# Optimization experiments

Measured on AMD Instinct MI355X. Metric: run time of the kernel, lower is better.

The kernel has to match this reference:

```python
import jax, jax.numpy as jnp
import numpy as np

S2_CH, DEM_CH, OUT_CH = 256, 64, 256
B, H, W = 4, 64, 64


def setup_inputs() -> dict:
    key = jax.random.key(0)
    ks = jax.random.split(key, 8)
    x_s2 = jax.random.normal(ks[0], (B, S2_CH, H, W), dtype=jnp.float32)
    x_dem = jax.random.normal(ks[1], (B, DEM_CH, H, W), dtype=jnp.float32)
    # 1x1 conv weights collapse to [out_ch, in_ch] matrices + bias
    Wq = jax.random.normal(ks[2], (OUT_CH, S2_CH), dtype=jnp.float32) * (S2_CH ** -0.5)
    bq = jnp.zeros((OUT_CH,), dtype=jnp.float32)
    Wk = jax.random.normal(ks[3], (OUT_CH, DEM_CH), dtype=jnp.float32) * (DEM_CH ** -0.5)
    bk = jnp.zeros((OUT_CH,), dtype=jnp.float32)
    Wv = jax.random.normal(ks[4], (OUT_CH, DEM_CH), dtype=jnp.float32) * (DEM_CH ** -0.5)
    bv = jnp.zeros((OUT_CH,), dtype=jnp.float32)
    return {"x_s2": x_s2, "x_dem": x_dem, "Wq": Wq, "bq": bq,
            "Wk": Wk, "bk": bk, "Wv": Wv, "bv": bv}


def reference(x_s2, x_dem, Wq, bq, Wk, bk, Wv, bv):
    b, c, h, w = x_s2.shape
    n = h * w
    xs = x_s2.reshape(b, c, n)                      # [b, s2_ch, n]
    xd = x_dem.reshape(b, x_dem.shape[1], n)        # [b, dem_ch, n]
    # 1x1 convs == per-pixel GEMMs
    q = jnp.einsum('oc,bcn->bon', Wq, xs) + bq[:, None]   # [b, out_ch, n]
    k = jnp.einsum('oc,bcn->bon', Wk, xd) + bk[:, None]   # [b, out_ch, n]
    v = jnp.einsum('oc,bcn->bon', Wv, xd) + bv[:, None]   # [b, out_ch, n]
    scale = q.shape[1] ** -0.5
    # attn[b,i,j] = softmax_j( k[b,:,i] . q[b,:,j] * scale )
    attn = jax.nn.softmax(jnp.einsum('bci,bcj->bij', k, q) * scale, axis=-1)
    out = jnp.einsum('bci,bij->bcj', v, attn).reshape(b, -1, h, w)
    return out + x_s2
```

## Files before the change

### kernel.cpp

```cpp
#include <hip/hip_runtime.h>
#include <hip/hip_bf16.h>
#include <cstdint>

#define B_  4
#define N_  4096
#define C_  256
#define CD_ 64

typedef unsigned short ushort_t;
typedef unsigned char uchar_t;
typedef __bf16 bf16x8 __attribute__((ext_vector_type(8)));
typedef float f32x4 __attribute__((ext_vector_type(4)));
typedef unsigned int u32x4 __attribute__((ext_vector_type(4)));

typedef const __attribute__((address_space(1))) void* gas_t;
typedef __attribute__((address_space(3))) void* las_t;

static constexpr float SCALE_LOG2E = 0.09016844005556021f;
static constexpr float SCALE_K8 = 0.3606737602222408f;
static constexpr float SCALE_Q8 = 0.25f;
static constexpr float VSCALE = 8192.0f;
static constexpr float VSCALE_INV = 1.0f / 8192.0f;

__device__ __forceinline__ ushort_t f2bf(float x) {
    union { float f; unsigned u; } v; v.f = x;
    unsigned u = v.u;
    unsigned r = (u + 0x7fffu + ((u >> 16) & 1u)) >> 16;
    return (ushort_t)r;
}

__device__ __forceinline__ uchar_t f2fp8(float x) {
    return (uchar_t)(__builtin_amdgcn_cvt_pk_fp8_f32(x, x, 0, false) & 0xff);
}

__device__ __forceinline__ bf16x8 ld_bf8(const ushort_t* p) {
    return *reinterpret_cast<const bf16x8*>(p);
}

__global__ __launch_bounds__(256, 4)
void proj_q_mfma(const float* __restrict__ X, const float* __restrict__ W,
                 const float* __restrict__ bias, ushort_t* __restrict__ dst,
                 uchar_t* __restrict__ dst8, int Cin) {
    __shared__ ushort_t sX[128][72];
    __shared__ ushort_t sW[64][72];
    const int tid = threadIdx.x;
    const int lane = tid & 63, g = lane >> 4, c16 = lane & 15;
    const int w = tid >> 6, wi = w >> 1, wj = w & 1;
    const int b = blockIdx.z, nb = blockIdx.x * 128, ob = blockIdx.y * 64;
    f32x4 acc[4][2];
#pragma unroll
    for (int nt = 0; nt < 4; ++nt)
#pragma unroll
        for (int ot = 0; ot < 2; ++ot) acc[nt][ot] = (f32x4){0.f, 0.f, 0.f, 0.f};

    const int cr = tid >> 5;
    const int n0 = (tid & 31) * 4;

    for (int k0 = 0; k0 < Cin; k0 += 64) {
#pragma unroll
        for (int p = 0; p < 8; ++p) {
            const int c = p * 8 + cr;
            float4 xv = *(const float4*)(X + ((size_t)b * Cin + k0 + c) * N_ + nb + n0);
            sX[n0 + 0][c] = f2bf(xv.x);
            sX[n0 + 1][c] = f2bf(xv.y);
            sX[n0 + 2][c] = f2bf(xv.z);
            sX[n0 + 3][c] = f2bf(xv.w);
        }
        {
            const int o = tid >> 2, cq = (tid & 3) * 16;
            const float* wsrc = W + (size_t)(ob + o) * Cin + k0 + cq;
            alignas(16) ushort_t tmp[16];
#pragma unroll
            for (int q = 0; q < 16; ++q) tmp[q] = f2bf(wsrc[q]);
            *(uint4*)&sW[o][cq]     = *(uint4*)&tmp[0];
            *(uint4*)&sW[o][cq + 8] = *(uint4*)&tmp[8];
        }
        __syncthreads();
#pragma unroll
        for (int ks = 0; ks < 2; ++ks) {
            bf16x8 af[4], bfr[2];
#pragma unroll
            for (int nt = 0; nt < 4; ++nt)
                af[nt] = *(const bf16x8*)&sX[wi * 64 + nt * 16 + c16][ks * 32 + g * 8];
#pragma unroll
            for (int ot = 0; ot < 2; ++ot)
                bfr[ot] = *(const bf16x8*)&sW[wj * 32 + ot * 16 + c16][ks * 32 + g * 8];
#pragma unroll
            for (int nt = 0; nt < 4; ++nt)
#pragma unroll
                for (int ot = 0; ot < 2; ++ot)
                    acc[nt][ot] = __builtin_amdgcn_mfma_f32_16x16x32_bf16(af[nt], bfr[ot], acc[nt][ot], 0, 0, 0);
        }
        __syncthreads();
    }
#pragma unroll
    for (int ot = 0; ot < 2; ++ot) {
        const int o = ob + wj * 32 + ot * 16 + c16;
        const float bia = bias[o];
#pragma unroll
        for (int nt = 0; nt < 4; ++nt) {
#pragma unroll
            for (int r = 0; r < 4; ++r) {
                const int n = nb + wi * 64 + nt * 16 + g * 4 + r;
                const float v = acc[nt][ot][r] + bia;
                if (dst8 != nullptr)
                    dst8[((size_t)b * N_ + n) * C_ + o] = f2fp8(v * SCALE_Q8);
                else
                    dst[((size_t)b * N_ + n) * C_ + o] = f2bf(v);
            }
        }
    }
}

__global__ __launch_bounds__(256, 4)
void proj_kv_mfma(const float* __restrict__ X, const float* __restrict__ Wk,
                  const float* __restrict__ bk, const float* __restrict__ Wv,
                  const float* __restrict__ bv, ushort_t* __restrict__ Kt,
                  uchar_t* __restrict__ Kt8, ushort_t* __restrict__ Vm) {
    __shared__ ushort_t sX[128][72];
    __shared__ ushort_t sWk[64][72];
    __shared__ ushort_t sWv[64][72];
    const int tid = threadIdx.x;
    const int lane = tid & 63, g = lane >> 4, c16 = lane & 15;
    const int w = tid >> 6;
    const int b = blockIdx.z, nb = blockIdx.x * 128, ob = blockIdx.y * 64;

    {
        const int cr = tid >> 5, n0 = (tid & 31) * 4;
#pragma unroll
        for (int p = 0; p < 8; ++p) {
            const int c = p * 8 + cr;
            float4 xv = *(const float4*)(X + ((size_t)b * CD_ + c) * N_ + nb + n0);
            sX[n0 + 0][c] = f2bf(xv.x);
            sX[n0 + 1][c] = f2bf(xv.y);
            sX[n0 + 2][c] = f2bf(xv.z);
            sX[n0 + 3][c] = f2bf(xv.w);
        }
        const int o = tid >> 2, cq = (tid & 3) * 16;
        alignas(16) ushort_t tk[16], tv[16];
        const float* ksrc = Wk + (size_t)(ob + o) * CD_ + cq;
        const float* vsrc = Wv + (size_t)(ob + o) * CD_ + cq;
#pragma unroll
        for (int q = 0; q < 16; ++q) { tk[q] = f2bf(ksrc[q]); tv[q] = f2bf(vsrc[q]); }
        *(uint4*)&sWk[o][cq]     = *(uint4*)&tk[0];
        *(uint4*)&sWk[o][cq + 8] = *(uint4*)&tk[8];
        *(uint4*)&sWv[o][cq]     = *(uint4*)&tv[0];
        *(uint4*)&sWv[o][cq + 8] = *(uint4*)&tv[8];
    }
    __syncthreads();
    {
        const int wi = w >> 1, wj = w & 1;
        f32x4 acc[4][2];
#pragma unroll
        for (int nt = 0; nt < 4; ++nt)
#pragma unroll
            for (int ot = 0; ot < 2; ++ot) acc[nt][ot] = (f32x4){0.f, 0.f, 0.f, 0.f};
#pragma unroll
        for (int ks = 0; ks < 2; ++ks) {
            bf16x8 af[4], bfr[2];
#pragma unroll
            for (int nt = 0; nt < 4; ++nt)
                af[nt] = *(const bf16x8*)&sX[wi * 64 + nt * 16 + c16][ks * 32 + g * 8];
#pragma unroll
            for (int ot = 0; ot < 2; ++ot)
                bfr[ot] = *(const bf16x8*)&sWk[wj * 32 + ot * 16 + c16][ks * 32 + g * 8];
#pragma unroll
            for (int nt = 0; nt < 4; ++nt)
#pragma unroll
                for (int ot = 0; ot < 2; ++ot)
                    acc[nt][ot] = __builtin_amdgcn_mfma_f32_16x16x32_bf16(af[nt], bfr[ot], acc[nt][ot], 0, 0, 0);
        }
#pragma unroll
        for (int ot = 0; ot < 2; ++ot) {
            const int o = ob + wj * 32 + ot * 16 + c16;
            const float bia = bk[o];
#pragma unroll
            for (int nt = 0; nt < 4; ++nt)
#pragma unroll
                for (int r = 0; r < 4; ++r) {
                    const int n = nb + wi * 64 + nt * 16 + g * 4 + r;
                    const float v = acc[nt][ot][r] + bia;
                    if (Kt8 != nullptr)
                        Kt8[((size_t)b * N_ + n) * C_ + o] = f2fp8(v * SCALE_K8);
                    else
                        Kt[((size_t)b * N_ + n) * C_ + o] = f2bf(v * SCALE_LOG2E);
                }
        }
    }
    {
        const int ow = w & 1, nw = w >> 1;
        f32x4 acc[2][4];
#pragma unroll
        for (int mt = 0; mt < 2; ++mt)
#pragma unroll
            for (int nt = 0; nt < 4; ++nt) acc[mt][nt] = (f32x4){0.f, 0.f, 0.f, 0.f};
#pragma unroll
        for (int ks = 0; ks < 2; ++ks) {
            bf16x8 af[2], bfr[4];
#pragma unroll
            for (int mt = 0; mt < 2; ++mt)
                af[mt] = *(const bf16x8*)&sWv[ow * 32 + mt * 16 + c16][ks * 32 + g * 8];
#pragma unroll
            for (int nt = 0; nt < 4; ++nt)
                bfr[nt] = *(const bf16x8*)&sX[nw * 64 + nt * 16 + c16][ks * 32 + g * 8];
#pragma unroll
            for (int mt = 0; mt < 2; ++mt)
#pragma unroll
                for (int nt = 0; nt < 4; ++nt)
                    acc[mt][nt] = __builtin_amdgcn_mfma_f32_16x16x32_bf16(af[mt], bfr[nt], acc[mt][nt], 0, 0, 0);
        }
#pragma unroll
        for (int mt = 0; mt < 2; ++mt) {
            const float4 bi4 = *(const float4*)(bv + ob + ow * 32 + mt * 16 + g * 4);
            const float bia[4] = {bi4.x, bi4.y, bi4.z, bi4.w};
#pragma unroll
            for (int nt = 0; nt < 4; ++nt) {
                const int n = nb + nw * 64 + nt * 16 + c16;
#pragma unroll
                for (int r = 0; r < 4; ++r) {
                    const int o = ob + ow * 32 + mt * 16 + g * 4 + r;
                    Vm[((size_t)b * C_ + o) * N_ + n] = f2bf(acc[mt][nt][r] + bia[r]);
                }
            }
        }
    }
}

__global__ __launch_bounds__(256, 4)
void stats_fp8_kernel(const uchar_t* __restrict__ Kt8, const uchar_t* __restrict__ Qt8,
                      uchar_t* __restrict__ PT8, float* __restrict__ lpart) {
    __shared__ uchar_t smem8[32768];
    uchar_t* sp8 = smem8;
    float* lsum = (float*)(smem8 + 18432);
    const int tid = threadIdx.x;
    const int lane = tid & 63, g = lane >> 4, c16 = lane & 15;
    const int w = tid >> 6, wi = w >> 1, wj = w & 1;
    const int b = blockIdx.z;
    const int ib = blockIdx.y * 128, jb = blockIdx.x * 128;
    f32x4 acc[4][4];
#pragma unroll
    for (int mt = 0; mt < 4; ++mt)
#pragma unroll
        for (int nt = 0; nt < 4; ++nt) acc[mt][nt] = (f32x4){0.f, 0.f, 0.f, 0.f};

    const int srow = tid >> 2;
    const int sc = tid & 3;

    auto stage = [&](int kc, int dbase) {
#pragma unroll
        for (int q = 0; q < 2; ++q) {
            const int row = q * 64 + srow;
            const int gc = sc ^ ((row >> 1) & 3);
            const uchar_t* srcA = Kt8 + ((size_t)(b * N_ + ib + row)) * C_ + kc * 64 + gc * 16;
            const uchar_t* srcB = Qt8 + ((size_t)(b * N_ + jb + row)) * C_ + kc * 64 + gc * 16;
            __builtin_amdgcn_global_load_lds((gas_t)srcA, (las_t)&smem8[dbase + (q * 256 + tid) * 16], 16, 0, 0);
            __builtin_amdgcn_global_load_lds((gas_t)srcB, (las_t)&smem8[dbase + 8192 + (q * 256 + tid) * 16], 16, 0, 0);
        }
    };

    stage(0, 0);
    __syncthreads();
    for (int t = 0; t < 4; ++t) {
        const int dbase = (t & 1) * 16384;
        if (t < 3) stage(t + 1, 16384 - dbase);
#pragma unroll
        for (int ks = 0; ks < 2; ++ks) {
            const int sp = ks * 2 + (g >> 1);
            const int bo = (g & 1) * 8;
            long af[4], bf[4];
#pragma unroll
            for (int mt = 0; mt < 4; ++mt) {
                const int row = wi * 64 + mt * 16 + c16;
                af[mt] = *(const long*)&smem8[dbase + row * 64 + ((sp ^ ((row >> 1) & 3)) * 16) + bo];
            }
#pragma unroll
            for (int nt = 0; nt < 4; ++nt) {
                const int row = wj * 64 + nt * 16 + c16;
                bf[nt] = *(const long*)&smem8[dbase + 8192 + row * 64 + ((sp ^ ((row >> 1) & 3)) * 16) + bo];
            }
#pragma unroll
            for (int mt = 0; mt < 4; ++mt)
#pragma unroll
                for (int nt = 0; nt < 4; ++nt)
                    acc[mt][nt] = __builtin_amdgcn_mfma_f32_16x16x32_fp8_fp8(af[mt], bf[nt], acc[mt][nt], 0, 0, 0);
        }
        __syncthreads();
    }
    const float sh = 3.0f;
#pragma unroll
    for (int mt = 0; mt < 4; ++mt) {
        float rs[4] = {0.f, 0.f, 0.f, 0.f};
#pragma unroll
        for (int nt = 0; nt < 4; ++nt) {
            float e0 = __builtin_amdgcn_exp2f(acc[mt][nt][0] - sh);
            float e1 = __builtin_amdgcn_exp2f(acc[mt][nt][1] - sh);
            float e2 = __builtin_amdgcn_exp2f(acc[mt][nt][2] - sh);
            float e3 = __builtin_amdgcn_exp2f(acc[mt][nt][3] - sh);
            rs[0] += e0; rs[1] += e1; rs[2] += e2; rs[3] += e3;
            int pk = __builtin_amdgcn_cvt_pk_fp8_f32(e0, e1, 0, false);
            pk = __builtin_amdgcn_cvt_pk_fp8_f32(e2, e3, pk, true);
            const int jl = wj * 64 + nt * 16 + c16;
            const int il = wi * 64 + mt * 16 + g * 4;
            *(int*)&sp8[jl * 144 + il] = pk;
        }
#pragma unroll
        for (int r = 0; r < 4; ++r) {
            float s = rs[r];
            s += __shfl_xor(s, 1, 64);
            s += __shfl_xor(s, 2, 64);
            s += __shfl_xor(s, 4, 64);
            s += __shfl_xor(s, 8, 64);
            if (c16 == 0)
                lsum[wj * 128 + wi * 64 + mt * 16 + g * 4 + r] = s;
        }
    }
    __syncthreads();
    {
        const int chb = tid & 7;
        const int rb = tid >> 3;
#pragma unroll
        for (int r = 0; r < 4; ++r) {
            const int jl = r * 32 + rb;
            u32x4 v = *(const u32x4*)&sp8[jl * 144 + chb * 16];
            __builtin_nontemporal_store(v,
                (u32x4*)(PT8 + ((size_t)(b * N_ + jb + jl)) * N_ + ib + chb * 16));
        }
        if (tid < 128) {
            float tot = lsum[tid] + lsum[128 + tid];
            lpart[((size_t)(b * 32 + (jb >> 7))) * N_ + ib + tid] = tot;
        }
    }
}

__global__ __launch_bounds__(256, 4)
void stats_kernel(const ushort_t* __restrict__ Kt, const ushort_t* __restrict__ Qt,
                  float* __restrict__ l) {
    __shared__ ushort_t smem[16384];
    uchar_t* smem8 = (uchar_t*)smem;
    const int tid = threadIdx.x;
    const int lane = tid & 63, g = lane >> 4, c16 = lane & 15;
    const int w = tid >> 6, wi = w >> 1, wj = w & 1;
    const int b = blockIdx.z;
    const int ib = blockIdx.y * 128, jb = blockIdx.x * 128;
    f32x4 acc[4][4];
#pragma unroll
    for (int mt = 0; mt < 4; ++mt)
#pragma unroll
        for (int nt = 0; nt < 4; ++nt) acc[mt][nt] = (f32x4){0.f, 0.f, 0.f, 0.f};

    const int srow = tid >> 2;
    const int sc = tid & 3;

    auto stage = [&](int kc, int dbase) {
#pragma unroll
        for (int q = 0; q < 2; ++q) {
            const int row = q * 64 + srow;
            const int gc = sc ^ ((row >> 1) & 3);
            const ushort_t* srcA = Kt + ((size_t)(b * N_ + ib + row)) * C_ + kc * 32 + gc * 8;
            const ushort_t* srcB = Qt + ((size_t)(b * N_ + jb + row)) * C_ + kc * 32 + gc * 8;
            __builtin_amdgcn_global_load_lds((gas_t)srcA, (las_t)&smem8[dbase + (q * 256 + tid) * 16], 16, 0, 0);
            __builtin_amdgcn_global_load_lds((gas_t)srcB, (las_t)&smem8[dbase + 8192 + (q * 256 + tid) * 16], 16, 0, 0);
        }
    };

    stage(0, 0);
    __syncthreads();
    for (int t = 0; t < 8; ++t) {
        const int dbase = (t & 1) * 16384;
        if (t < 7) stage(t + 1, 16384 - dbase);
        bf16x8 af[4], bf[4];
#pragma unroll
        for (int mt = 0; mt < 4; ++mt) {
            const int row = wi * 64 + mt * 16 + c16;
            af[mt] = *(const bf16x8*)&smem8[dbase + row * 64 + ((g ^ ((row >> 1) & 3)) * 16)];
        }
#pragma unroll
        for (int nt = 0; nt < 4; ++nt) {
            const int row = wj * 64 + nt * 16 + c16;
            bf[nt] = *(const bf16x8*)&smem8[dbase + 8192 + row * 64 + ((g ^ ((row >> 1) & 3)) * 16)];
        }
#pragma unroll
        for (int mt = 0; mt < 4; ++mt)
#pragma unroll
            for (int nt = 0; nt < 4; ++nt)
                acc[mt][nt] = __builtin_amdgcn_mfma_f32_16x16x32_bf16(af[mt], bf[nt], acc[mt][nt], 0, 0, 0);
        __syncthreads();
    }
#pragma unroll
    for (int mt = 0; mt < 4; ++mt) {
        float rs[4] = {0.f, 0.f, 0.f, 0.f};
#pragma unroll
        for (int nt = 0; nt < 4; ++nt) {
            rs[0] += __builtin_amdgcn_exp2f(acc[mt][nt][0]);
            rs[1] += __builtin_amdgcn_exp2f(acc[mt][nt][1]);
            rs[2] += __builtin_amdgcn_exp2f(acc[mt][nt][2]);
            rs[3] += __builtin_amdgcn_exp2f(acc[mt][nt][3]);
        }
#pragma unroll
        for (int r = 0; r < 4; ++r) {
            float s = rs[r];
            s += __shfl_xor(s, 1, 64);
            s += __shfl_xor(s, 2, 64);
            s += __shfl_xor(s, 4, 64);
            s += __shfl_xor(s, 8, 64);
            if (c16 == 0)
                atomicAdd(l + (size_t)b * N_ + ib + wi * 64 + mt * 16 + g * 4 + r, s);
        }
    }
}

__global__ void reduce_l_kernel(const float* __restrict__ lpart, float* __restrict__ l) {
    const int b = blockIdx.y;
    const int i = (blockIdx.x * 256 + threadIdx.x) * 4;
    float4 s = {0.f, 0.f, 0.f, 0.f};
#pragma unroll
    for (int jt = 0; jt < 32; ++jt) {
        float4 p = *(const float4*)(lpart + ((size_t)(b * 32 + jt)) * N_ + i);
        s.x += p.x; s.y += p.y; s.z += p.z; s.w += p.w;
    }
    *(float4*)(l + (size_t)b * N_ + i) = s;
}

__global__ void scale_v_kernel(const ushort_t* __restrict__ Vm, const float* __restrict__ l,
                               uchar_t* __restrict__ Vs) {
    const int i = (blockIdx.x * 256 + threadIdx.x) * 8;
    const int c = blockIdx.y, b = blockIdx.z;
    float4 l0 = *(const float4*)(l + (size_t)b * N_ + i);
    float4 l1 = *(const float4*)(l + (size_t)b * N_ + i + 4);
    float r[8] = {__builtin_amdgcn_rcpf(l0.x), __builtin_amdgcn_rcpf(l0.y),
                  __builtin_amdgcn_rcpf(l0.z), __builtin_amdgcn_rcpf(l0.w),
                  __builtin_amdgcn_rcpf(l1.x), __builtin_amdgcn_rcpf(l1.y),
                  __builtin_amdgcn_rcpf(l1.z), __builtin_amdgcn_rcpf(l1.w)};
    const size_t off = ((size_t)(b * C_ + c)) * N_ + i;
    uint4 v = *(const uint4*)(Vm + off);
    unsigned vw[4] = {v.x, v.y, v.z, v.w};
    float f[8];
#pragma unroll
    for (int q = 0; q < 4; ++q) {
        union { unsigned u; float fl; } lo, hi;
        lo.u = (vw[q] & 0xffffu) << 16;
        hi.u = vw[q] & 0xffff0000u;
        f[q * 2 + 0] = lo.fl * r[q * 2 + 0] * VSCALE;
        f[q * 2 + 1] = hi.fl * r[q * 2 + 1] * VSCALE;
    }
    int d0 = __builtin_amdgcn_cvt_pk_fp8_f32(f[0], f[1], 0, false);
    d0 = __builtin_amdgcn_cvt_pk_fp8_f32(f[2], f[3], d0, true);
    int d1 = __builtin_amdgcn_cvt_pk_fp8_f32(f[4], f[5], 0, false);
    d1 = __builtin_amdgcn_cvt_pk_fp8_f32(f[6], f[7], d1, true);
    uint2 o; o.x = (unsigned)d0; o.y = (unsigned)d1;
    *(uint2*)(Vs + off) = o;
}

__global__ __launch_bounds__(512, 4)
void gemm_out2_kernel(const uchar_t* __restrict__ A ,
                      const uchar_t* __restrict__ Bm ,
                      const float* __restrict__ R ,
                      float* __restrict__ out) {
    __shared__ uchar_t smem[73728];
    const int tid = threadIdx.x;
    const int lane = tid & 63, g = lane >> 4, c16 = lane & 15;
    const int w = tid >> 6;
    const int cw = w * 32;
    const int b = blockIdx.y;
    const int jb = blockIdx.x * 32;

    f32x4 acc[2][2];
#pragma unroll
    for (int mt = 0; mt < 2; ++mt)
#pragma unroll
        for (int nt = 0; nt < 2; ++nt) acc[mt][nt] = (f32x4){0.f, 0.f, 0.f, 0.f};

    const int sch = tid & 7;

    auto stage = [&](int k0, int dbase) {
#pragma unroll
        for (int q = 0; q < 4; ++q) {
            const int slot = q * 512 + tid;
            const int row = slot >> 3;
            const int gc = sch ^ (row & 7);
            const uchar_t* src = A + ((size_t)(b * C_ + row)) * N_ + k0 + gc * 16;
            __builtin_amdgcn_global_load_lds((gas_t)src, (las_t)&smem[dbase + slot * 16], 16, 0, 0);
        }
        if (tid < 256) {
            const int row = tid >> 3;
            const int gc = sch ^ (row & 7);
            const uchar_t* src = Bm + ((size_t)(b * N_ + jb + row)) * N_ + k0 + gc * 16;
            __builtin_amdgcn_global_load_lds((gas_t)src, (las_t)&smem[dbase + 32768 + tid * 16], 16, 0, 2);
        }
    };

    stage(0, 0);
    __syncthreads();
    for (int t = 0; t < 32; ++t) {
        const int dbase = (t & 1) * 36864;
        if (t < 31) stage((t + 1) * 128, 36864 - dbase);
        const uchar_t* sA = &smem[dbase];
        const uchar_t* sB = &smem[dbase + 32768];
#pragma unroll
        for (int ks = 0; ks < 4; ++ks) {
            const int lc = ks * 2 + (g >> 1);
            const int bo = (g & 1) * 8;
            long af[2], bfg[2];
#pragma unroll
            for (int mt = 0; mt < 2; ++mt) {
                const int row = cw + mt * 16 + c16;
                af[mt] = *(const long*)&sA[row * 128 + ((lc ^ (row & 7)) * 16) + bo];
            }
#pragma unroll
            for (int nt = 0; nt < 2; ++nt) {
                const int row = nt * 16 + c16;
                bfg[nt] = *(const long*)&sB[row * 128 + ((lc ^ (row & 7)) * 16) + bo];
            }
#pragma unroll
            for (int mt = 0; mt < 2; ++mt)
#pragma unroll
                for (int nt = 0; nt < 2; ++nt)
                    acc[mt][nt] = __builtin_amdgcn_mfma_f32_16x16x32_fp8_fp8(af[mt], bfg[nt], acc[mt][nt], 0, 0, 0);
        }
        __syncthreads();
    }
#pragma unroll
    for (int mt = 0; mt < 2; ++mt)
#pragma unroll
        for (int r = 0; r < 4; ++r) {
            const int c = cw + mt * 16 + g * 4 + r;
            const size_t rowoff = ((size_t)(b * C_ + c)) * N_ + jb;
#pragma unroll
            for (int nt = 0; nt < 2; ++nt) {
                const int j = nt * 16 + c16;
                float rv = __builtin_nontemporal_load(&R[rowoff + j]);
                __builtin_nontemporal_store(rv + acc[mt][nt][r] * VSCALE_INV,
                                            &out[rowoff + j]);
            }
        }
}

__global__ __launch_bounds__(512, 4)
void out_kernel(const ushort_t* __restrict__ Kt, const ushort_t* __restrict__ Qt,
                const ushort_t* __restrict__ V, const float* __restrict__ l,
                float* __restrict__ dout) {
    __shared__ ushort_t sQ[64][264];
    __shared__ ushort_t sP[64][264];
    const int tid = threadIdx.x;
    const int w = tid >> 6, lane = tid & 63, g = lane >> 4, c16 = lane & 15;
    const int b = blockIdx.z;
    const int jb = blockIdx.x * 64;
    const int ibase = blockIdx.y * 2048;
    {
        const int jl = tid >> 3, cp = (tid & 7) * 32;
        const ushort_t* src = Qt + ((size_t)(b * N_ + jb + jl)) * C_ + cp;
        uint4 a0 = *(const uint4*)(src);
        uint4 a1 = *(const uint4*)(src + 8);
        uint4 a2 = *(const uint4*)(src + 16);
        uint4 a3 = *(const uint4*)(src + 24);
        *(uint4*)&sQ[jl][cp + 0]  = a0;
        *(uint4*)&sQ[jl][cp + 8]  = a1;
        *(uint4*)&sQ[jl][cp + 16] = a2;
        *(uint4*)&sQ[jl][cp + 24] = a3;
    }
    f32x4 acc[2][4];
#pragma unroll
    for (int mt = 0; mt < 2; ++mt)
#pragma unroll
        for (int nt = 0; nt < 4; ++nt) acc[mt][nt] = (f32x4){0.f, 0.f, 0.f, 0.f};

    const int bw = w * 32;

    for (int ic = 0; ic < 8; ++ic) {
        const int i0 = ibase + ic * 256;
        float rv[2][4];
#pragma unroll
        for (int mt = 0; mt < 2; ++mt) {
            float4 lr = *(const float4*)(l + (size_t)b * N_ + i0 + bw + mt * 16 + g * 4);
            rv[mt][0] = __builtin_amdgcn_logf(lr.x);
            rv[mt][1] = __builtin_amdgcn_logf(lr.y);
            rv[mt][2] = __builtin_amdgcn_logf(lr.z);
            rv[mt][3] = __builtin_amdgcn_logf(lr.w);
        }
        __syncthreads();
        f32x4 sa[2][4];
#pragma unroll
        for (int mt = 0; mt < 2; ++mt)
#pragma unroll
            for (int nt = 0; nt < 4; ++nt) sa[mt][nt] = (f32x4){0.f, 0.f, 0.f, 0.f};
#pragma unroll
        for (int k = 0; k < 8; ++k) {
            bf16x8 av[2];
#pragma unroll
            for (int mt = 0; mt < 2; ++mt)
                av[mt] = ld_bf8(Kt + ((size_t)(b * N_ + i0 + bw + mt * 16 + c16)) * C_ + k * 32 + g * 8);
#pragma unroll
            for (int nt = 0; nt < 4; ++nt) {
                bf16x8 bv = *(const bf16x8*)&sQ[nt * 16 + c16][k * 32 + g * 8];
#pragma unroll
                for (int mt = 0; mt < 2; ++mt)
                    sa[mt][nt] = __builtin_amdgcn_mfma_f32_16x16x32_bf16(av[mt], bv, sa[mt][nt], 0, 0, 0);
            }
        }
#pragma unroll
        for (int mt = 0; mt < 2; ++mt)
#pragma unroll
            for (int nt = 0; nt < 4; ++nt) {
                const int j = nt * 16 + c16;
                unsigned p0 = f2bf(__builtin_amdgcn_exp2f(sa[mt][nt][0] - rv[mt][0]));
                unsigned p1 = f2bf(__builtin_amdgcn_exp2f(sa[mt][nt][1] - rv[mt][1]));
                unsigned p2 = f2bf(__builtin_amdgcn_exp2f(sa[mt][nt][2] - rv[mt][2]));
                unsigned p3 = f2bf(__builtin_amdgcn_exp2f(sa[mt][nt][3] - rv[mt][3]));
                uint2 pk; pk.x = p0 | (p1 << 16); pk.y = p2 | (p3 << 16);
                *(uint2*)&sP[j][bw + mt * 16 + g * 4] = pk;
            }
        __syncthreads();
#pragma unroll
        for (int ks = 0; ks < 8; ++ks) {
            bf16x8 va[2];
#pragma unroll
            for (int mt = 0; mt < 2; ++mt)
                va[mt] = ld_bf8(V + ((size_t)(b * C_ + bw + mt * 16 + c16)) * N_ + i0 + ks * 32 + g * 8);
#pragma unroll
            for (int nt = 0; nt < 4; ++nt) {
                bf16x8 pb = *(const bf16x8*)&sP[nt * 16 + c16][ks * 32 + g * 8];
#pragma unroll
                for (int mt = 0; mt < 2; ++mt)
                    acc[mt][nt] = __builtin_amdgcn_mfma_f32_16x16x32_bf16(va[mt], pb, acc[mt][nt], 0, 0, 0);
            }
        }
    }
#pragma unroll
    for (int mt = 0; mt < 2; ++mt)
#pragma unroll
        for (int nt = 0; nt < 4; ++nt)
#pragma unroll
            for (int r = 0; r < 4; ++r) {
                const int c = bw + mt * 16 + g * 4 + r;
                const int j = jb + nt * 16 + c16;
                atomicAdd(dout + ((size_t)b * C_ + c) * N_ + j, acc[mt][nt][r]);
            }
}

extern "C" void kernel_launch(void* const* d_in, const int* in_sizes, int n_in,
                              void* d_out, int out_size, void* d_ws, size_t ws_size,
                              hipStream_t stream) {
    const float* x_s2  = (const float*)d_in[0];
    const float* x_dem = (const float*)d_in[1];
    const float* Wq = (const float*)d_in[2];
    const float* bq = (const float*)d_in[3];
    const float* Wk = (const float*)d_in[4];
    const float* bk = (const float*)d_in[5];
    const float* Wv = (const float*)d_in[6];
    const float* bv = (const float*)d_in[7];
    float* out = (float*)d_out;

    const size_t MiB = 1024 * 1024;
    char* ws = (char*)d_ws;
    ushort_t* Qt = (ushort_t*)(ws);
    uchar_t*  Qt8 = (uchar_t*)(ws);
    ushort_t* Kt = (ushort_t*)(ws + 8  * MiB);
    uchar_t*  Kt8 = (uchar_t*)(ws + 8 * MiB);
    ushort_t* Vm = (ushort_t*)(ws + 16 * MiB);
    uchar_t*  Vs = (uchar_t*) (ws + 24 * MiB);
    float*    lp = (float*)   (ws + 24 * MiB);
    float*    lv = (float*)   (ws + 28 * MiB);
    uchar_t*  PT = (uchar_t*) (ws + 29 * MiB);
    const bool bigws = ws_size >= 93 * MiB;

    if (!bigws) {
        hipMemsetAsync(lv, 0, (size_t)B_ * N_ * sizeof(float), stream);
        hipMemcpyAsync(out, x_s2, (size_t)B_ * C_ * N_ * sizeof(float),
                       hipMemcpyDeviceToDevice, stream);
    }

    proj_q_mfma<<<dim3(N_ / 128, C_ / 64, B_), 256, 0, stream>>>(
        x_s2, Wq, bq, Qt, bigws ? Qt8 : (uchar_t*)nullptr, C_);
    proj_kv_mfma<<<dim3(N_ / 128, C_ / 64, B_), 256, 0, stream>>>(
        x_dem, Wk, bk, Wv, bv, Kt, bigws ? Kt8 : (uchar_t*)nullptr, Vm);
    if (bigws) {
        stats_fp8_kernel<<<dim3(N_ / 128, N_ / 128, B_), 256, 0, stream>>>(Kt8, Qt8, PT, lp);
        reduce_l_kernel<<<dim3(N_ / 1024, B_), 256, 0, stream>>>(lp, lv);
        scale_v_kernel<<<dim3(N_ / 2048, C_, B_), 256, 0, stream>>>(Vm, lv, Vs);
        gemm_out2_kernel<<<dim3(N_ / 32, B_), 512, 0, stream>>>(Vs, PT, x_s2, out);
    } else {
        stats_kernel<<<dim3(N_ / 128, N_ / 128, B_), 256, 0, stream>>>(Kt, Qt, lv);
        out_kernel<<<dim3(N_ / 64, 2, B_), 512, 0, stream>>>(Kt, Qt, Vm, lv, out);
    }
}
```

Baseline: 198.7 us.

## Permute K-dimension byte order in fp8 operands to enable 16-byte LDS fragment reads

The fp8 Q, K, P and V tensors are now written with their reduction-dimension bytes permuted so that each lane's two consecutive MFMA k-steps sit in one contiguous 16-byte chunk. The score and output GEMMs then issue one 128-bit LDS read per fragment pair instead of two 64-bit reads, halving the LDS read instruction count. The producers (projection epilogues, softmax P store, V scaling) must apply matching permutations, and any mismatch would silently corrupt the result.

```diff
diff --git a/kernel.cpp b/kernel.cpp
--- a/kernel.cpp
+++ b/kernel.cpp
@@ -12,6 +12,7 @@
 typedef __bf16 bf16x8 __attribute__((ext_vector_type(8)));
 typedef float f32x4 __attribute__((ext_vector_type(4)));
 typedef unsigned int u32x4 __attribute__((ext_vector_type(4)));
+typedef long longx2 __attribute__((ext_vector_type(2)));
 
 typedef const __attribute__((address_space(1))) void* gas_t;
 typedef __attribute__((address_space(3))) void* las_t;
@@ -35,6 +36,13 @@
 
 __device__ __forceinline__ bf16x8 ld_bf8(const ushort_t* p) {
     return *reinterpret_cast<const bf16x8*>(p);
+}
+
+__device__ __forceinline__ int perm16(int s) {
+    return (((s & 3) | ((s >> 1) & 4)) << 4) | ((s & 4) << 1);
+}
+__device__ __forceinline__ int perm8(int s) {
+    return ((s & 3) << 4) | ((s & 4) << 1);
 }
 
 __global__ __launch_bounds__(256, 4)
@@ -97,6 +105,7 @@
     for (int ot = 0; ot < 2; ++ot) {
         const int o = ob + wj * 32 + ot * 16 + c16;
         const float bia = bias[o];
+        const int o_p = (o & ~63) | perm8((o >> 3) & 7) | (o & 7);
 #pragma unroll
         for (int nt = 0; nt < 4; ++nt) {
 #pragma unroll
@@ -104,7 +113,7 @@
                 const int n = nb + wi * 64 + nt * 16 + g * 4 + r;
                 const float v = acc[nt][ot][r] + bia;
                 if (dst8 != nullptr)
-                    dst8[((size_t)b * N_ + n) * C_ + o] = f2fp8(v * SCALE_Q8);
+                    dst8[((size_t)b * N_ + n) * C_ + o_p] = f2fp8(v * SCALE_Q8);
                 else
                     dst[((size_t)b * N_ + n) * C_ + o] = f2bf(v);
             }
@@ -174,6 +183,7 @@
         for (int ot = 0; ot < 2; ++ot) {
             const int o = ob + wj * 32 + ot * 16 + c16;
             const float bia = bk[o];
+            const int o_p = (o & ~63) | perm8((o >> 3) & 7) | (o & 7);
 #pragma unroll
             for (int nt = 0; nt < 4; ++nt)
 #pragma unroll
@@ -181,7 +191,7 @@
                     const int n = nb + wi * 64 + nt * 16 + g * 4 + r;
                     const float v = acc[nt][ot][r] + bia;
                     if (Kt8 != nullptr)
-                        Kt8[((size_t)b * N_ + n) * C_ + o] = f2fp8(v * SCALE_K8);
+                        Kt8[((size_t)b * N_ + n) * C_ + o_p] = f2fp8(v * SCALE_K8);
                     else
                         Kt[((size_t)b * N_ + n) * C_ + o] = f2bf(v * SCALE_LOG2E);
                 }
@@ -263,27 +273,24 @@
     for (int t = 0; t < 4; ++t) {
         const int dbase = (t & 1) * 16384;
         if (t < 3) stage(t + 1, 16384 - dbase);
-#pragma unroll
-        for (int ks = 0; ks < 2; ++ks) {
-            const int sp = ks * 2 + (g >> 1);
-            const int bo = (g & 1) * 8;
-            long af[4], bf[4];
-#pragma unroll
-            for (int mt = 0; mt < 4; ++mt) {
-                const int row = wi * 64 + mt * 16 + c16;
-                af[mt] = *(const long*)&smem8[dbase + row * 64 + ((sp ^ ((row >> 1) & 3)) * 16) + bo];
-            }
-#pragma unroll
-            for (int nt = 0; nt < 4; ++nt) {
-                const int row = wj * 64 + nt * 16 + c16;
-                bf[nt] = *(const long*)&smem8[dbase + 8192 + row * 64 + ((sp ^ ((row >> 1) & 3)) * 16) + bo];
-            }
+        longx2 a2[4], b2[4];
+#pragma unroll
+        for (int mt = 0; mt < 4; ++mt) {
+            const int row = wi * 64 + mt * 16 + c16;
+            a2[mt] = *(const longx2*)&smem8[dbase + row * 64 + ((g ^ ((row >> 1) & 3)) * 16)];
+        }
+#pragma unroll
+        for (int nt = 0; nt < 4; ++nt) {
+            const int row = wj * 64 + nt * 16 + c16;
+            b2[nt] = *(const longx2*)&smem8[dbase + 8192 + row * 64 + ((g ^ ((row >> 1) & 3)) * 16)];
+        }
+#pragma unroll
+        for (int ks = 0; ks < 2; ++ks)
 #pragma unroll
             for (int mt = 0; mt < 4; ++mt)
 #pragma unroll
                 for (int nt = 0; nt < 4; ++nt)
-                    acc[mt][nt] = __builtin_amdgcn_mfma_f32_16x16x32_fp8_fp8(af[mt], bf[nt], acc[mt][nt], 0, 0, 0);
-        }
+                    acc[mt][nt] = __builtin_amdgcn_mfma_f32_16x16x32_fp8_fp8(a2[mt][ks], b2[nt][ks], acc[mt][nt], 0, 0, 0);
         __syncthreads();
     }
     const float sh = 3.0f;
@@ -301,7 +308,8 @@
             pk = __builtin_amdgcn_cvt_pk_fp8_f32(e2, e3, pk, true);
             const int jl = wj * 64 + nt * 16 + c16;
             const int il = wi * 64 + mt * 16 + g * 4;
-            *(int*)&sp8[jl * 144 + il] = pk;
+            const int il_p = perm16(il >> 3) | (il & 7);
+            *(int*)&sp8[jl * 144 + il_p] = pk;
         }
 #pragma unroll
         for (int r = 0; r < 4; ++r) {
@@ -448,7 +456,8 @@
     int d1 = __builtin_amdgcn_cvt_pk_fp8_f32(f[4], f[5], 0, false);
     d1 = __builtin_amdgcn_cvt_pk_fp8_f32(f[6], f[7], d1, true);
     uint2 o; o.x = (unsigned)d0; o.y = (unsigned)d1;
-    *(uint2*)(Vs + off) = o;
+    const int i_p = (i & ~127) | perm16((i >> 3) & 15);
+    *(uint2*)(Vs + ((size_t)(b * C_ + c)) * N_ + i_p) = o;
 }
 
 __global__ __launch_bounds__(512, 4)
@@ -496,27 +505,28 @@
         if (t < 31) stage((t + 1) * 128, 36864 - dbase);
         const uchar_t* sA = &smem[dbase];
         const uchar_t* sB = &smem[dbase + 32768];
-#pragma unroll
-        for (int ks = 0; ks < 4; ++ks) {
-            const int lc = ks * 2 + (g >> 1);
-            const int bo = (g & 1) * 8;
-            long af[2], bfg[2];
+        longx2 a2[2][2], b2[2][2];
+#pragma unroll
+        for (int p = 0; p < 2; ++p) {
 #pragma unroll
             for (int mt = 0; mt < 2; ++mt) {
                 const int row = cw + mt * 16 + c16;
-                af[mt] = *(const long*)&sA[row * 128 + ((lc ^ (row & 7)) * 16) + bo];
+                a2[mt][p] = *(const longx2*)&sA[row * 128 + (((p * 4 + g) ^ (row & 7)) * 16)];
             }
 #pragma unroll
             for (int nt = 0; nt < 2; ++nt) {
                 const int row = nt * 16 + c16;
-                bfg[nt] = *(const long*)&sB[row * 128 + ((lc ^ (row & 7)) * 16) + bo];
-            }
+                b2[nt][p] = *(const longx2*)&sB[row * 128 + (((p * 4 + g) ^ (row & 7)) * 16)];
+            }
+        }
+#pragma unroll
+        for (int ks = 0; ks < 4; ++ks)
 #pragma unroll
             for (int mt = 0; mt < 2; ++mt)
 #pragma unroll
                 for (int nt = 0; nt < 2; ++nt)
-                    acc[mt][nt] = __builtin_amdgcn_mfma_f32_16x16x32_fp8_fp8(af[mt], bfg[nt], acc[mt][nt], 0, 0, 0);
-        }
+                    acc[mt][nt] = __builtin_amdgcn_mfma_f32_16x16x32_fp8_fp8(
+                        a2[mt][ks >> 1][ks & 1], b2[nt][ks >> 1][ks & 1], acc[mt][nt], 0, 0, 0);
         __syncthreads();
     }
 #pragma unroll
```

Result: faster. 193.7 us (-2.5%).
